# Kernel tuning notes

Hardware: AMD Instinct MI355X
Metric: run time of the kernel (lower is better)

The kernel has to match this reference:

```python
import jax, jax.numpy as jnp
import numpy as np

N_NODES = 100000
N_EDGES = 3200000
D_IN = 128
D_HID = 128
D_FF = 256
N_CLASSES = 26
N_GRAPHS = 512


def setup_inputs() -> dict:
    key = jax.random.key(0)
    ks = jax.random.split(key, 12)
    s = 0.05
    return {
        "x": jax.random.normal(ks[0], (N_NODES, D_IN), dtype=jnp.float32),
        "edge_index": jax.random.randint(ks[1], (2, N_EDGES), 0, N_NODES, dtype=jnp.int64),
        "batch": jnp.sort(jax.random.randint(ks[2], (N_NODES,), 0, N_GRAPHS, dtype=jnp.int64)),
        "W1": jax.random.normal(ks[3], (D_IN, D_HID), dtype=jnp.float32) * s,
        "b1": jnp.zeros((D_HID,), dtype=jnp.float32),
        "W2": jax.random.normal(ks[4], (D_HID, D_HID), dtype=jnp.float32) * s,
        "b2": jnp.zeros((D_HID,), dtype=jnp.float32),
        "W3": jax.random.normal(ks[5], (D_HID, D_HID), dtype=jnp.float32) * s,
        "b3": jnp.zeros((D_HID,), dtype=jnp.float32),
        "Wfc": jax.random.normal(ks[6], (D_HID, D_FF), dtype=jnp.float32) * s,
        "bfc": jnp.zeros((D_FF,), dtype=jnp.float32),
        "Wfc2": jax.random.normal(ks[7], (D_FF, N_CLASSES), dtype=jnp.float32) * s,
        "bfc2": jnp.zeros((N_CLASSES,), dtype=jnp.float32),
    }


def _gcn_layer(x, src, dst, norm, W, b):
    # GCNConv: h = x @ W; out[dst] += norm_e * h[src]; out += b
    h = x @ W                                   # [N, D]
    msg = h[src] * norm[:, None]                # [E+N, D] gather + scale
    agg = jax.ops.segment_sum(msg, dst, num_segments=N_NODES)
    return agg + b


def reference(x, edge_index, batch, W1, b1, W2, b2, W3, b3, Wfc, bfc, Wfc2, bfc2):
    # add self-loops (PyG GCNConv default) and compute symmetric normalization once
    loop = jnp.arange(N_NODES, dtype=edge_index.dtype)
    src = jnp.concatenate([edge_index[0], loop])
    dst = jnp.concatenate([edge_index[1], loop])
    deg = jax.ops.segment_sum(jnp.ones_like(dst, dtype=x.dtype), dst, num_segments=N_NODES)
    dinv = jnp.where(deg > 0, jax.lax.rsqrt(deg), 0.0)
    norm = dinv[src] * dinv[dst]               # D^{-1/2} A_hat D^{-1/2}

    h = jax.nn.relu(_gcn_layer(x, src, dst, norm, W1, b1))
    h = jax.nn.relu(_gcn_layer(h, src, dst, norm, W2, b2))
    h = jax.nn.relu(_gcn_layer(h, src, dst, norm, W3, b3))

    # global mean pool over graphs
    sums = jax.ops.segment_sum(h, batch, num_segments=N_GRAPHS)       # [G, D]
    cnts = jax.ops.segment_sum(jnp.ones((h.shape[0],), h.dtype), batch, num_segments=N_GRAPHS)
    pooled = sums / jnp.maximum(cnts, 1.0)[:, None]

    out = jax.nn.relu(pooled @ Wfc + bfc)       # dropout is identity at inference
    return out @ Wfc2 + bfc2                    # [G, num_classes]
```

## Files before the change

### kernel.cpp

```cpp
#include <hip/hip_runtime.h>
#include <hip/hip_bf16.h>

typedef __bf16 bf16;
typedef __attribute__((ext_vector_type(8))) __bf16 bf16x8;
typedef __attribute__((ext_vector_type(4))) float f32x4;

constexpr int N_NODES   = 100000;
constexpr int N_PAD     = 100032;
constexpr int D         = 128;
constexpr int D_FF      = 256;
constexpr int N_CLASSES = 26;
constexpr int N_GRAPHS  = 512;
constexpr int NB1       = 256;
constexpr int NBUCK     = (N_NODES + 511) / 512;

__device__ inline float2 bf2f(unsigned u) {
    float lo = __uint_as_float(u << 16);
    float hi = __uint_as_float(u & 0xffff0000u);
    return make_float2(lo, hi);
}


__global__ __launch_bounds__(1024) void p1misc_kernel(const int* __restrict__ edst,
                                                      int* __restrict__ gcount, int e,
                                                      const int* __restrict__ batch,
                                                      int* __restrict__ starts, int n,
                                                      const float* __restrict__ W0,
                                                      const float* __restrict__ W1,
                                                      const float* __restrict__ W2,
                                                      bf16* __restrict__ WT3,
                                                      float* __restrict__ gsum) {
    int t = threadIdx.x;
    if (blockIdx.x < NB1) {
        __shared__ int cnt[NBUCK];
        for (int q = t; q < NBUCK; q += 1024) cnt[q] = 0;
        __syncthreads();
        int chunk = (e + NB1 - 1) / NB1;
        int lo = blockIdx.x * chunk;
        int hi = min(e, lo + chunk);
        for (int i = lo + t; i < hi; i += 1024)
            atomicAdd(&cnt[edst[i] >> 9], 1);
        __syncthreads();
        for (int q = t; q < NBUCK; q += 1024)
            gcount[q * NB1 + blockIdx.x] = cnt[q];
    } else {
        int mb = blockIdx.x - NB1;
        if (mb == 0) {
            if (t <= N_GRAPHS) {
                int lo = 0, hi = n;
                while (lo < hi) {
                    int mid = (lo + hi) >> 1;
                    if (batch[mid] < t) lo = mid + 1; else hi = mid;
                }
                starts[t] = lo;
            }
        } else if (mb <= 48) {
            int idx = (mb - 1) * 1024 + t;
            int l = idx >> 14;
            int rem = idx & 16383;
            int nn = rem >> 7;
            int kk = rem & 127;
            const float* W = (l == 0) ? W0 : (l == 1) ? W1 : W2;
            WT3[idx] = (bf16)W[kk * D + nn];
        } else {
            int idx = (mb - 49) * 1024 + t;
            f32x4 z = {0.f, 0.f, 0.f, 0.f};
            *((f32x4*)gsum + idx) = z;
        }
    }
}

__global__ __launch_bounds__(256) void scan1(const int* __restrict__ in,
                                             int* out, int* bsum, int n) {
    __shared__ int sd[256];
    int i = blockIdx.x * 256 + threadIdx.x;
    int v = (i < n) ? in[i] : 0;
    sd[threadIdx.x] = v; __syncthreads();
    for (int off = 1; off < 256; off <<= 1) {
        int t = (threadIdx.x >= off) ? sd[threadIdx.x - off] : 0;
        __syncthreads();
        sd[threadIdx.x] += t;
        __syncthreads();
    }
    if (i < n) out[i] = sd[threadIdx.x] - v;
    if (threadIdx.x == 255) bsum[blockIdx.x] = sd[255];
}

__global__ __launch_bounds__(1024) void scan2k(const int* __restrict__ bsum,
                                               int* __restrict__ boff, int nb) {
    __shared__ int sd[1024];
    int t = threadIdx.x;
    int v = (t < nb) ? bsum[t] : 0;
    sd[t] = v; __syncthreads();
    for (int off = 1; off < 1024; off <<= 1) {
        int x = (t >= off) ? sd[t - off] : 0;
        __syncthreads();
        sd[t] += x;
        __syncthreads();
    }
    if (t < nb) boff[t] = sd[t] - v;
}

__global__ __launch_bounds__(1024) void p3_scatter(const int* __restrict__ esrc,
                                                   const int* __restrict__ edst,
                                                   const int* __restrict__ gbase,
                                                   const int* __restrict__ boff,
                                                   int* __restrict__ ebuf, int e) {
    __shared__ int cur[NBUCK];
    for (int t = threadIdx.x; t < NBUCK; t += 1024)
        cur[t] = gbase[t * NB1 + blockIdx.x] + boff[t];
    __syncthreads();
    int chunk = (e + NB1 - 1) / NB1;
    int lo = blockIdx.x * chunk;
    int hi = min(e, lo + chunk);
    for (int i = lo + threadIdx.x; i < hi; i += 1024) {
        int d = edst[i], s = esrc[i];
        int pos = atomicAdd(&cur[d >> 9], 1);
        ebuf[pos] = (s << 9) | (d & 511);
    }
}

__global__ __launch_bounds__(1024) void p45_fill(const int* __restrict__ ebuf,
                                                 const int* __restrict__ gbase,
                                                 const int* __restrict__ boff,
                                                 float* __restrict__ dinv,
                                                 int* __restrict__ rowptr,
                                                 int* __restrict__ csrc, int e, int n) {
    __shared__ int cnt[512];
    __shared__ int ps[512];
    __shared__ int cur[512];
    int b = blockIdx.x, t = threadIdx.x;
    if (t < 512) cnt[t] = 0;
    __syncthreads();
    int lo = gbase[b * NB1] + boff[b];
    int hi = (b + 1 < NBUCK) ? gbase[(b + 1) * NB1] + boff[b + 1] : e;
    for (int i = lo + t; i < hi; i += 1024)
        atomicAdd(&cnt[ebuf[i] & 511], 1);
    __syncthreads();
    int a = (t < 512) ? cnt[t] : 0;
    if (t < 512) ps[t] = a;
    __syncthreads();
    for (int off = 1; off < 512; off <<= 1) {
        int v = (t >= off && t < 512) ? ps[t - off] : 0;
        __syncthreads();
        if (t < 512) ps[t] += v;
        __syncthreads();
    }
    if (t < 512) {
        int g0 = lo + ps[t] - a;
        int node = b * 512 + t;
        cur[t] = g0;
        if (node < n) {
            rowptr[node] = g0;
            dinv[node] = 1.0f / sqrtf((float)(a + 1));
        }
    }
    if (b == 0 && t == 0) rowptr[n] = e;
    __syncthreads();
    for (int i = lo + t; i < hi; i += 1024) {
        int pe = ebuf[i];
        int pos = atomicAdd(&cur[pe & 511], 1);
        csrc[pos] = pe >> 9;
    }
}


__global__ __launch_bounds__(256) void gemm_f32_kernel(const float* __restrict__ A,
                                                       const bf16* __restrict__ WT,
                                                       bf16* __restrict__ C,
                                                       const float* __restrict__ dinv, int n) {
    int wave = threadIdx.x >> 6;
    int lane = threadIdx.x & 63;
    int m16  = lane & 15;
    int quad = lane >> 4;
    int row0 = blockIdx.x * 64 + wave * 16;
    int arowi = row0 + m16;

    bf16x8 a[4];
    const float* arow = A + (size_t)arowi * D + quad * 8;
#pragma unroll
    for (int kt = 0; kt < 4; ++kt) {
        float4 f0 = make_float4(0.f, 0.f, 0.f, 0.f);
        float4 f1 = make_float4(0.f, 0.f, 0.f, 0.f);
        if (arowi < n) {
            f0 = *(const float4*)(arow + kt * 32);
            f1 = *(const float4*)(arow + kt * 32 + 4);
        }
        bf16x8 v = { (bf16)f0.x, (bf16)f0.y, (bf16)f0.z, (bf16)f0.w,
                     (bf16)f1.x, (bf16)f1.y, (bf16)f1.z, (bf16)f1.w };
        a[kt] = v;
    }

    float sc[4];
#pragma unroll
    for (int r = 0; r < 4; ++r) {
        int rr = row0 + quad * 4 + r;
        sc[r] = (rr < n) ? dinv[rr] : 0.f;
    }

#pragma unroll
    for (int nt = 0; nt < 8; ++nt) {
        f32x4 acc = {0.f, 0.f, 0.f, 0.f};
        const bf16* brow = WT + (nt * 16 + m16) * D + quad * 8;
#pragma unroll
        for (int kt = 0; kt < 4; ++kt) {
            bf16x8 b = *(const bf16x8*)(brow + kt * 32);
            acc = __builtin_amdgcn_mfma_f32_16x16x32_bf16(a[kt], b, acc, 0, 0, 0);
        }
#pragma unroll
        for (int r = 0; r < 4; ++r)
            C[(row0 + quad * 4 + r) * D + nt * 16 + m16] = (bf16)(sc[r] * acc[r]);
    }
}

__device__ inline void agg_node(const bf16* __restrict__ h, int v, int n, int c,
                                const int* __restrict__ rowptr,
                                const int* __restrict__ csrc,
                                const float* __restrict__ dinv,
                                float& dv, float acc[8]) {
    int s = 0, e = 0;
    dv = 0.f;
    if (v < n) { s = rowptr[v]; e = rowptr[v + 1]; dv = dinv[v]; }
#pragma unroll
    for (int d = 0; d < 8; ++d) acc[d] = 0.f;
    if (v < n) {
        uint4 u = *(const uint4*)(h + (size_t)v * D + c * 8);
        float2 f0 = bf2f(u.x), f1 = bf2f(u.y), f2 = bf2f(u.z), f3 = bf2f(u.w);
        acc[0] = f0.x; acc[1] = f0.y; acc[2] = f1.x; acc[3] = f1.y;
        acc[4] = f2.x; acc[5] = f2.y; acc[6] = f3.x; acc[7] = f3.y;
    }
    int j = s;
    for (; j + 3 < e; j += 4) {
        int s0 = csrc[j], s1 = csrc[j + 1], s2 = csrc[j + 2], s3 = csrc[j + 3];
        uint4 u0 = *(const uint4*)(h + (size_t)s0 * D + c * 8);
        uint4 u1 = *(const uint4*)(h + (size_t)s1 * D + c * 8);
        uint4 u2 = *(const uint4*)(h + (size_t)s2 * D + c * 8);
        uint4 u3 = *(const uint4*)(h + (size_t)s3 * D + c * 8);
        {
            float2 a0 = bf2f(u0.x), a1 = bf2f(u0.y), a2 = bf2f(u0.z), a3 = bf2f(u0.w);
            acc[0] += a0.x; acc[1] += a0.y; acc[2] += a1.x; acc[3] += a1.y;
            acc[4] += a2.x; acc[5] += a2.y; acc[6] += a3.x; acc[7] += a3.y;
        }
        {
            float2 a0 = bf2f(u1.x), a1 = bf2f(u1.y), a2 = bf2f(u1.z), a3 = bf2f(u1.w);
            acc[0] += a0.x; acc[1] += a0.y; acc[2] += a1.x; acc[3] += a1.y;
            acc[4] += a2.x; acc[5] += a2.y; acc[6] += a3.x; acc[7] += a3.y;
        }
        {
            float2 a0 = bf2f(u2.x), a1 = bf2f(u2.y), a2 = bf2f(u2.z), a3 = bf2f(u2.w);
            acc[0] += a0.x; acc[1] += a0.y; acc[2] += a1.x; acc[3] += a1.y;
            acc[4] += a2.x; acc[5] += a2.y; acc[6] += a3.x; acc[7] += a3.y;
        }
        {
            float2 a0 = bf2f(u3.x), a1 = bf2f(u3.y), a2 = bf2f(u3.z), a3 = bf2f(u3.w);
            acc[0] += a0.x; acc[1] += a0.y; acc[2] += a1.x; acc[3] += a1.y;
            acc[4] += a2.x; acc[5] += a2.y; acc[6] += a3.x; acc[7] += a3.y;
        }
    }
    for (; j < e; ++j) {
        int s0 = csrc[j];
        uint4 u0 = *(const uint4*)(h + (size_t)s0 * D + c * 8);
        float2 a0 = bf2f(u0.x), a1 = bf2f(u0.y), a2 = bf2f(u0.z), a3 = bf2f(u0.w);
        acc[0] += a0.x; acc[1] += a0.y; acc[2] += a1.x; acc[3] += a1.y;
        acc[4] += a2.x; acc[5] += a2.y; acc[6] += a3.x; acc[7] += a3.y;
    }
}

__global__ __launch_bounds__(256) void spmm_gemm_kernel(const bf16* __restrict__ h,
                                                        const int* __restrict__ rowptr,
                                                        const int* __restrict__ csrc,
                                                        const float* __restrict__ dinv,
                                                        const float* __restrict__ bias,
                                                        const bf16* __restrict__ WT,
                                                        bf16* __restrict__ C, int n) {
    __shared__ bf16 tile[16][136];
    int t = threadIdx.x;
    int grp = t >> 4;
    int c   = t & 15;
    int v   = blockIdx.x * 16 + grp;
    float dv, acc[8];
    agg_node(h, v, n, c, rowptr, csrc, dinv, dv, acc);
    {
        float4 bi0 = *(const float4*)(bias + c * 8);
        float4 bi1 = *(const float4*)(bias + c * 8 + 4);
        bf16x8 o;
        o[0] = (bf16)fmaxf(fmaf(dv, acc[0], bi0.x), 0.f);
        o[1] = (bf16)fmaxf(fmaf(dv, acc[1], bi0.y), 0.f);
        o[2] = (bf16)fmaxf(fmaf(dv, acc[2], bi0.z), 0.f);
        o[3] = (bf16)fmaxf(fmaf(dv, acc[3], bi0.w), 0.f);
        o[4] = (bf16)fmaxf(fmaf(dv, acc[4], bi1.x), 0.f);
        o[5] = (bf16)fmaxf(fmaf(dv, acc[5], bi1.y), 0.f);
        o[6] = (bf16)fmaxf(fmaf(dv, acc[6], bi1.z), 0.f);
        o[7] = (bf16)fmaxf(fmaf(dv, acc[7], bi1.w), 0.f);
        *(bf16x8*)(&tile[grp][c * 8]) = o;
    }
    __syncthreads();

    int wave = t >> 6, lane = t & 63;
    int m16 = lane & 15, quad = lane >> 4;
    bf16x8 a[4];
#pragma unroll
    for (int kt = 0; kt < 4; ++kt)
        a[kt] = *(const bf16x8*)(&tile[m16][quad * 8 + kt * 32]);

    int base = blockIdx.x * 16;
    float sc[4];
#pragma unroll
    for (int r = 0; r < 4; ++r) {
        int rr = base + quad * 4 + r;
        sc[r] = (rr < n) ? dinv[rr] : 0.f;
    }

#pragma unroll
    for (int nt2 = 0; nt2 < 2; ++nt2) {
        int nt = wave * 2 + nt2;
        f32x4 accq = {0.f, 0.f, 0.f, 0.f};
        const bf16* brow = WT + (nt * 16 + m16) * D + quad * 8;
#pragma unroll
        for (int kt = 0; kt < 4; ++kt) {
            bf16x8 b = *(const bf16x8*)(brow + kt * 32);
            accq = __builtin_amdgcn_mfma_f32_16x16x32_bf16(a[kt], b, accq, 0, 0, 0);
        }
#pragma unroll
        for (int r = 0; r < 4; ++r)
            C[(size_t)(base + quad * 4 + r) * D + nt * 16 + m16] = (bf16)(sc[r] * accq[r]);
    }
}

__global__ __launch_bounds__(256) void spmm2_pool_kernel(const bf16* __restrict__ h,
                                                         const int* __restrict__ rowptr,
                                                         const int* __restrict__ csrc,
                                                         const float* __restrict__ dinv,
                                                         const float* __restrict__ bias,
                                                         const int* __restrict__ batch,
                                                         float* __restrict__ gsum, int n) {
    __shared__ float tile[16][D];
    __shared__ int gid[16];
    int t = threadIdx.x;
    int grp = t >> 4;
    int c   = t & 15;
    int v   = blockIdx.x * 16 + grp;
    float dv, acc[8];
    agg_node(h, v, n, c, rowptr, csrc, dinv, dv, acc);
    float4 bi0 = *(const float4*)(bias + c * 8);
    float4 bi1 = *(const float4*)(bias + c * 8 + 4);
    float r0 = fmaxf(fmaf(dv, acc[0], bi0.x), 0.f);
    float r1 = fmaxf(fmaf(dv, acc[1], bi0.y), 0.f);
    float r2 = fmaxf(fmaf(dv, acc[2], bi0.z), 0.f);
    float r3 = fmaxf(fmaf(dv, acc[3], bi0.w), 0.f);
    float r4 = fmaxf(fmaf(dv, acc[4], bi1.x), 0.f);
    float r5 = fmaxf(fmaf(dv, acc[5], bi1.y), 0.f);
    float r6 = fmaxf(fmaf(dv, acc[6], bi1.z), 0.f);
    float r7 = fmaxf(fmaf(dv, acc[7], bi1.w), 0.f);
    if (v >= n) { r0 = r1 = r2 = r3 = r4 = r5 = r6 = r7 = 0.f; }
    tile[grp][c * 8 + 0] = r0; tile[grp][c * 8 + 1] = r1;
    tile[grp][c * 8 + 2] = r2; tile[grp][c * 8 + 3] = r3;
    tile[grp][c * 8 + 4] = r4; tile[grp][c * 8 + 5] = r5;
    tile[grp][c * 8 + 6] = r6; tile[grp][c * 8 + 7] = r7;
    if (c == 0) gid[grp] = (v < n) ? batch[v] : -1;
    __syncthreads();
    if (t < D) {
        int curg = gid[0];
        float sum = 0.f;
        if (curg >= 0) {
#pragma unroll 1
            for (int k = 0; k < 16; ++k) {
                int gg = gid[k];
                if (gg < 0) break;
                if (gg != curg) {
                    atomicAdd(&gsum[(size_t)curg * D + t], sum);
                    curg = gg; sum = 0.f;
                }
                sum += tile[k][t];
            }
            atomicAdd(&gsum[(size_t)curg * D + t], sum);
        }
    }
}

__global__ __launch_bounds__(256) void fc_head_kernel(const float* __restrict__ gsum,
                                                      const int* __restrict__ starts,
                                                      const float* __restrict__ Wfc,
                                                      const float* __restrict__ bfc,
                                                      const float* __restrict__ Wfc2,
                                                      const float* __restrict__ bfc2,
                                                      float* __restrict__ out) {
    __shared__ float pr[D];
    __shared__ float hid[D_FF];
    __shared__ float red[N_CLASSES][9];
    int g = blockIdx.x, t = threadIdx.x;
    if (t < D) {
        float ccount = fmaxf((float)(starts[g + 1] - starts[g]), 1.0f);
        pr[t] = gsum[(size_t)g * D + t] / ccount;
    }
    __syncthreads();
    float a0 = 0.f, a1 = 0.f, a2 = 0.f, a3 = 0.f;
    for (int k = 0; k < D; k += 4) {
        a0 = fmaf(pr[k],     Wfc[k * D_FF + t],       a0);
        a1 = fmaf(pr[k + 1], Wfc[(k + 1) * D_FF + t], a1);
        a2 = fmaf(pr[k + 2], Wfc[(k + 2) * D_FF + t], a2);
        a3 = fmaf(pr[k + 3], Wfc[(k + 3) * D_FF + t], a3);
    }
    hid[t] = fmaxf((a0 + a1) + (a2 + a3) + bfc[t], 0.f);
    __syncthreads();
    if (t < N_CLASSES * 8) {
        int cls = t >> 3, kk = t & 7;
        float o = 0.f;
        for (int k = kk; k < D_FF; k += 8)
            o = fmaf(hid[k], Wfc2[k * N_CLASSES + cls], o);
        red[cls][kk] = o;
    }
    __syncthreads();
    if (t < N_CLASSES) {
        float o = bfc2[t];
#pragma unroll
        for (int k = 0; k < 8; ++k) o += red[t][k];
        out[g * N_CLASSES + t] = o;
    }
}


extern "C" void kernel_launch(void* const* d_in, const int* in_sizes, int n_in,
                              void* d_out, int out_size, void* d_ws, size_t ws_size,
                              hipStream_t stream) {
    const float* x     = (const float*)d_in[0];
    const int*   eidx  = (const int*)d_in[1];
    const int*   batch = (const int*)d_in[2];
    const float* W[3]  = { (const float*)d_in[3], (const float*)d_in[5], (const float*)d_in[7] };
    const float* b[3]  = { (const float*)d_in[4], (const float*)d_in[6], (const float*)d_in[8] };
    const float* Wfc   = (const float*)d_in[9];
    const float* bfc   = (const float*)d_in[10];
    const float* Wfc2  = (const float*)d_in[11];
    const float* bfc2  = (const float*)d_in[12];
    float* out = (float*)d_out;

    const int E = in_sizes[1] / 2;
    const int N = in_sizes[0] / D;
    const int* esrc = eidx;
    const int* edst = eidx + E;

    uint8_t* base = (uint8_t*)d_ws;
    size_t off = 0;
    auto alloc = [&](size_t bytes) -> void* {
        void* p = base + off;
        off = (off + bytes + 255) & ~(size_t)255;
        return p;
    };
    bf16*  hA     = (bf16*) alloc((size_t)N_PAD * D * 2);
    bf16*  hB     = (bf16*) alloc((size_t)N_PAD * D * 2);
    bf16*  WT3    = (bf16*) alloc((size_t)3 * D * D * 2);
    int*   csrc   = (int*)  alloc((size_t)E * 4);
    int*   ebuf   = (int*)  alloc((size_t)E * 4);
    int*   gcount = (int*)  alloc((size_t)NBUCK * NB1 * 4);
    int*   gbase  = (int*)  alloc((size_t)(NBUCK * NB1 + 1) * 4);
    int*   rowptr = (int*)  alloc((size_t)(N + 1) * 4);
    float* dinv   = (float*)alloc((size_t)N * 4);
    int*   bsum   = (int*)  alloc(4096);
    int*   boff   = (int*)  alloc(4096);
    int*   starts = (int*)  alloc((size_t)(N_GRAPHS + 1) * 4);
    float* gsum   = (float*)alloc((size_t)N_GRAPHS * D * 4);
    (void)ws_size; (void)n_in; (void)out_size;

    const int GB  = N_PAD / 64;
    const int SGB = (N + 15) / 16;
    const int GCN = NBUCK * NB1;
    const int GCB = (GCN + 255) / 256;

    p1misc_kernel<<<NB1 + 65, 1024, 0, stream>>>(edst, gcount, E, batch, starts, N,
                                                 W[0], W[1], W[2], WT3, gsum);
    scan1<<<GCB, 256, 0, stream>>>(gcount, gbase, bsum, GCN);
    scan2k<<<1, 1024, 0, stream>>>(bsum, boff, GCB);
    p3_scatter<<<NB1, 1024, 0, stream>>>(esrc, edst, gbase, boff, ebuf, E);
    p45_fill<<<NBUCK, 1024, 0, stream>>>(ebuf, gbase, boff, dinv, rowptr, csrc, E, N);

    gemm_f32_kernel<<<GB, 256, 0, stream>>>(x, WT3, hA, dinv, N);
    spmm_gemm_kernel<<<SGB, 256, 0, stream>>>(hA, rowptr, csrc, dinv, b[0],
                                              WT3 + (size_t)1 * D * D, hB, N);
    spmm_gemm_kernel<<<SGB, 256, 0, stream>>>(hB, rowptr, csrc, dinv, b[1],
                                              WT3 + (size_t)2 * D * D, hA, N);
    spmm2_pool_kernel<<<SGB, 256, 0, stream>>>(hA, rowptr, csrc, dinv, b[2],
                                               batch, gsum, N);

    fc_head_kernel<<<N_GRAPHS, 256, 0, stream>>>(gsum, starts, Wfc, bfc, Wfc2, bfc2, out);
}
```

Before: 574.4 us.

## Fold global prefix scan into scatter and fill kernels, dropping two launches

Removes the separate two-level scan kernels over the bucket-by-block count matrix. Each scatter block now recomputes bucket totals and its own per-block prefix from the raw counts, and each fill block recomputes its bucket's start and end by block reductions. This saves two kernel launches and their serialization points. In exchange it adds redundant reads of the count matrix: every scatter block reads all of it, and fill blocks read a prefix of it whose length grows with the bucket index.

```diff
diff --git a/kernel.cpp b/kernel.cpp
--- a/kernel.cpp
+++ b/kernel.cpp
@@ -70,70 +70,74 @@
     }
 }
 
-__global__ __launch_bounds__(256) void scan1(const int* __restrict__ in,
-                                             int* out, int* bsum, int n) {
-    __shared__ int sd[256];
-    int i = blockIdx.x * 256 + threadIdx.x;
-    int v = (i < n) ? in[i] : 0;
-    sd[threadIdx.x] = v; __syncthreads();
-    for (int off = 1; off < 256; off <<= 1) {
-        int t = (threadIdx.x >= off) ? sd[threadIdx.x - off] : 0;
-        __syncthreads();
-        sd[threadIdx.x] += t;
-        __syncthreads();
-    }
-    if (i < n) out[i] = sd[threadIdx.x] - v;
-    if (threadIdx.x == 255) bsum[blockIdx.x] = sd[255];
-}
-
-__global__ __launch_bounds__(1024) void scan2k(const int* __restrict__ bsum,
-                                               int* __restrict__ boff, int nb) {
-    __shared__ int sd[1024];
-    int t = threadIdx.x;
-    int v = (t < nb) ? bsum[t] : 0;
-    sd[t] = v; __syncthreads();
-    for (int off = 1; off < 1024; off <<= 1) {
-        int x = (t >= off) ? sd[t - off] : 0;
-        __syncthreads();
-        sd[t] += x;
-        __syncthreads();
-    }
-    if (t < nb) boff[t] = sd[t] - v;
-}
-
-__global__ __launch_bounds__(1024) void p3_scatter(const int* __restrict__ esrc,
+__global__ __launch_bounds__(1024) void p3_scatter(const int* __restrict__ gcount,
+                                                   const int* __restrict__ esrc,
                                                    const int* __restrict__ edst,
-                                                   const int* __restrict__ gbase,
-                                                   const int* __restrict__ boff,
                                                    int* __restrict__ ebuf, int e) {
     __shared__ int cur[NBUCK];
-    for (int t = threadIdx.x; t < NBUCK; t += 1024)
-        cur[t] = gbase[t * NB1 + blockIdx.x] + boff[t];
+    __shared__ int tot[NBUCK];
+    int t = threadIdx.x;
+    int b = blockIdx.x;
+    if (t < NBUCK) {
+        int sum = 0, part = 0;
+        const int* row = gcount + t * NB1;
+        for (int c = 0; c < NB1; ++c) {
+            int v = row[c];
+            sum += v;
+            part += (c < b) ? v : 0;
+        }
+        tot[t] = sum;
+        cur[t] = part;
+    }
+    __syncthreads();
+    for (int off = 1; off < NBUCK; off <<= 1) {
+        int v = (t >= off && t < NBUCK) ? tot[t - off] : 0;
+        __syncthreads();
+        if (t < NBUCK) tot[t] += v;
+        __syncthreads();
+    }
+    if (t < NBUCK) cur[t] += (t > 0) ? tot[t - 1] : 0;
     __syncthreads();
     int chunk = (e + NB1 - 1) / NB1;
-    int lo = blockIdx.x * chunk;
+    int lo = b * chunk;
     int hi = min(e, lo + chunk);
-    for (int i = lo + threadIdx.x; i < hi; i += 1024) {
+    for (int i = lo + t; i < hi; i += 1024) {
         int d = edst[i], s = esrc[i];
         int pos = atomicAdd(&cur[d >> 9], 1);
         ebuf[pos] = (s << 9) | (d & 511);
     }
 }
 
-__global__ __launch_bounds__(1024) void p45_fill(const int* __restrict__ ebuf,
-                                                 const int* __restrict__ gbase,
-                                                 const int* __restrict__ boff,
+__global__ __launch_bounds__(1024) void p45_fill(const int* __restrict__ gcount,
+                                                 const int* __restrict__ ebuf,
                                                  float* __restrict__ dinv,
                                                  int* __restrict__ rowptr,
                                                  int* __restrict__ csrc, int e, int n) {
+    __shared__ int red[1024];
     __shared__ int cnt[512];
     __shared__ int ps[512];
     __shared__ int cur[512];
     int b = blockIdx.x, t = threadIdx.x;
+    int s1 = 0;
+    for (int idx = t; idx < b * NB1; idx += 1024) s1 += gcount[idx];
+    red[t] = s1; __syncthreads();
+#pragma unroll
+    for (int off = 512; off > 0; off >>= 1) {
+        if (t < off) red[t] += red[t + off];
+        __syncthreads();
+    }
+    int lo = red[0];
+    __syncthreads();
+    red[t] = (t < NB1) ? gcount[b * NB1 + t] : 0; __syncthreads();
+#pragma unroll
+    for (int off = 512; off > 0; off >>= 1) {
+        if (t < off) red[t] += red[t + off];
+        __syncthreads();
+    }
+    int hi = lo + red[0];
+    __syncthreads();
     if (t < 512) cnt[t] = 0;
     __syncthreads();
-    int lo = gbase[b * NB1] + boff[b];
-    int hi = (b + 1 < NBUCK) ? gbase[(b + 1) * NB1] + boff[b + 1] : e;
     for (int i = lo + t; i < hi; i += 1024)
         atomicAdd(&cnt[ebuf[i] & 511], 1);
     __syncthreads();
@@ -452,26 +456,19 @@
     int*   csrc   = (int*)  alloc((size_t)E * 4);
     int*   ebuf   = (int*)  alloc((size_t)E * 4);
     int*   gcount = (int*)  alloc((size_t)NBUCK * NB1 * 4);
-    int*   gbase  = (int*)  alloc((size_t)(NBUCK * NB1 + 1) * 4);
     int*   rowptr = (int*)  alloc((size_t)(N + 1) * 4);
     float* dinv   = (float*)alloc((size_t)N * 4);
-    int*   bsum   = (int*)  alloc(4096);
-    int*   boff   = (int*)  alloc(4096);
     int*   starts = (int*)  alloc((size_t)(N_GRAPHS + 1) * 4);
     float* gsum   = (float*)alloc((size_t)N_GRAPHS * D * 4);
     (void)ws_size; (void)n_in; (void)out_size;
 
     const int GB  = N_PAD / 64;
     const int SGB = (N + 15) / 16;
-    const int GCN = NBUCK * NB1;
-    const int GCB = (GCN + 255) / 256;
 
     p1misc_kernel<<<NB1 + 65, 1024, 0, stream>>>(edst, gcount, E, batch, starts, N,
                                                  W[0], W[1], W[2], WT3, gsum);
-    scan1<<<GCB, 256, 0, stream>>>(gcount, gbase, bsum, GCN);
-    scan2k<<<1, 1024, 0, stream>>>(bsum, boff, GCB);
-    p3_scatter<<<NB1, 1024, 0, stream>>>(esrc, edst, gbase, boff, ebuf, E);
-    p45_fill<<<NBUCK, 1024, 0, stream>>>(ebuf, gbase, boff, dinv, rowptr, csrc, E, N);
+    p3_scatter<<<NB1, 1024, 0, stream>>>(gcount, esrc, edst, ebuf, E);
+    p45_fill<<<NBUCK, 1024, 0, stream>>>(gcount, ebuf, dinv, rowptr, csrc, E, N);
 
     gemm_f32_kernel<<<GB, 256, 0, stream>>>(x, WT3, hA, dinv, N);
     spmm_gemm_kernel<<<SGB, 256, 0, stream>>>(hA, rowptr, csrc, dinv, b[0],
```

After: 574.0 us. About the same (-0.1%).
